# Kernel tuning notes

Measured on AMD Instinct MI355X. Metric: run time of the kernel, lower is better.

The kernel has to match this reference:

```python
import jax, jax.numpy as jnp
import numpy as np

B, T, C = 2, 512, 256
HID = 4 * C
EPS = 1e-5

def _ln(z, g, b):
    mu = z.mean(-1, keepdims=True)
    var = z.var(-1, keepdims=True)
    return (z - mu) / jnp.sqrt(var + EPS) * g + b

def setup_inputs() -> dict:
    key = jax.random.key(0)
    ks = jax.random.split(key, 12)
    s = 0.02
    return {
        'x':   jax.random.normal(ks[0], (B, T, C), dtype=jnp.float32),
        'Wt':  jax.random.normal(ks[1], (C * C, C), dtype=jnp.float32) * s,   # transformation weight (no bias)
        'Wp':  jax.random.normal(ks[2], (C, C), dtype=jnp.float32) * s,       # proj weight
        'bp':  jnp.zeros((C,), dtype=jnp.float32),
        'g1':  jnp.ones((C,), dtype=jnp.float32),
        'b1':  jnp.zeros((C,), dtype=jnp.float32),
        'g2':  jnp.ones((C,), dtype=jnp.float32),
        'b2':  jnp.zeros((C,), dtype=jnp.float32),
        'W1':  jax.random.normal(ks[3], (HID, C), dtype=jnp.float32) * s,     # ffwd first linear
        'bf1': jnp.zeros((HID,), dtype=jnp.float32),
        'W2':  jax.random.normal(ks[4], (C, HID), dtype=jnp.float32) * s,     # ffwd second linear
        'bf2': jnp.zeros((C,), dtype=jnp.float32),
    }

def reference(x, Wt, Wp, bp, g1, b1, g2, b2, W1, bf1, W2, bf2):
    Bs, Ts, Cs = x.shape
    # ---- self-attention branch (pre-LN) ----
    h = _ln(x, g1, b1)
    # transformation: (B,T,C) @ (C, C^2) -> (B,T,C,C); faithfully multiplied by 0 as in source
    transform = (h @ Wt.T).reshape(Bs, Ts, Cs, Cs) * 0.0
    # einsum 'bcij,btj->btcj': contract over i (dim of size C)
    out = jnp.einsum('bcij,btj->btcj', transform, h)  # (B,T,T,C)
    tril = jnp.tril(jnp.ones((Ts, Ts), dtype=bool))
    out = jnp.where(tril[None, :, :, None], out, 0.0)
    out = out.sum(axis=2)  # (B,T,C)
    sa = out @ Wp.T + bp   # proj (dropout=0.0 -> identity)
    x = x + sa
    # ---- feed-forward branch (pre-LN) ----
    h2 = _ln(x, g2, b2)
    ff = jax.nn.relu(h2 @ W1.T + bf1) @ W2.T + bf2
    return x + ff
```

## Files before the change

kernel.cpp:

```cpp
#include <hip/hip_runtime.h>


typedef short bf8_t __attribute__((ext_vector_type(8)));
typedef float f4_t  __attribute__((ext_vector_type(4)));

__device__ inline unsigned short f2bf(float f) {
  unsigned u = __float_as_uint(f);
  u += 0x7fffu + ((u >> 16) & 1u);
  return (unsigned short)(u >> 16);
}

__global__ __launch_bounds__(256) void prep_kernel(
    const float* __restrict__ x, const float* __restrict__ bp,
    const float* __restrict__ g2, const float* __restrict__ b2,
    const float* __restrict__ W1, const float* __restrict__ W2,
    float* __restrict__ xp, unsigned short* __restrict__ h2,
    unsigned short* __restrict__ w1b, unsigned short* __restrict__ w2b) {
  const int b = blockIdx.x, t = threadIdx.x;
  if (b < 1024) {
    const int idx = (b << 8) + t;
    float v = x[idx] + bp[t];
    float s = v, s2 = v * v;
    #pragma unroll
    for (int off = 32; off > 0; off >>= 1) {
      s  += __shfl_down(s, off);
      s2 += __shfl_down(s2, off);
    }
    __shared__ float red[8];
    const int wave = t >> 6, lane = t & 63;
    if (lane == 0) { red[wave] = s; red[4 + wave] = s2; }
    __syncthreads();
    const float ts  = red[0] + red[1] + red[2] + red[3];
    const float ts2 = red[4] + red[5] + red[6] + red[7];
    const float mu   = ts * (1.0f / 256.0f);
    const float var  = ts2 * (1.0f / 256.0f) - mu * mu;
    const float rstd = rsqrtf(var + 1e-5f);
    xp[idx] = v;
    h2[idx] = f2bf((v - mu) * rstd * g2[t] + b2[t]);
  } else {
    const int e = ((b - 1024) << 10) + (t << 2);
    const float* src; unsigned short* dst;
    if (e < 262144) { src = W1 + e;          dst = w1b + e; }
    else            { src = W2 + (e - 262144); dst = w2b + (e - 262144); }
    const float4 v = *(const float4*)src;
    ushort4 o;
    o.x = f2bf(v.x); o.y = f2bf(v.y); o.z = f2bf(v.z); o.w = f2bf(v.w);
    *(ushort4*)dst = o;
  }
}

__global__ __launch_bounds__(256) void gemm1_kernel(
    const unsigned short* __restrict__ A,
    const unsigned short* __restrict__ Bm,
    const float* __restrict__ bias,
    unsigned short* __restrict__ H) {
  __shared__ unsigned short As[64 * 136];
  __shared__ unsigned short Bs[64 * 136];
  const int tid = threadIdx.x;
  const int bm = blockIdx.y << 6, bn = blockIdx.x << 6;
  const int wave = tid >> 6, lane = tid & 63;
  const int wy = (wave >> 1) << 5, wx = (wave & 1) << 5;
  const int quad = lane >> 4, l16 = lane & 15;
  f4_t acc[2][2] = {};

  for (int kt = 0; kt < 256; kt += 128) {
    #pragma unroll
    for (int c = 0; c < 4; ++c) {
      const int ch = (c << 8) + tid;
      const int r = ch >> 4, cc = ch & 15;
      *(uint4*)&As[r * 136 + (cc << 3)] =
          *(const uint4*)&A[((bm + r) << 8) + kt + (cc << 3)];
      *(uint4*)&Bs[r * 136 + (cc << 3)] =
          *(const uint4*)&Bm[((bn + r) << 8) + kt + (cc << 3)];
    }
    __syncthreads();
    #pragma unroll
    for (int ks = 0; ks < 4; ++ks) {
      bf8_t af[2], bv[2];
      #pragma unroll
      for (int i = 0; i < 2; ++i)
        af[i] = *(const bf8_t*)&As[(wy + (i << 4) + l16) * 136 + (ks << 5) + (quad << 3)];
      #pragma unroll
      for (int j = 0; j < 2; ++j)
        bv[j] = *(const bf8_t*)&Bs[(wx + (j << 4) + l16) * 136 + (ks << 5) + (quad << 3)];
      #pragma unroll
      for (int i = 0; i < 2; ++i)
        #pragma unroll
        for (int j = 0; j < 2; ++j)
          acc[i][j] = __builtin_amdgcn_mfma_f32_16x16x32_bf16(af[i], bv[j], acc[i][j], 0, 0, 0);
    }
    __syncthreads();
  }

  #pragma unroll
  for (int j = 0; j < 2; ++j) {
    const int n = bn + wx + (j << 4) + l16;
    const float bvv = bias[n];
    #pragma unroll
    for (int i = 0; i < 2; ++i) {
      #pragma unroll
      for (int r = 0; r < 4; ++r) {
        const int m = bm + wy + (i << 4) + (quad << 2) + r;
        float v = acc[i][j][r] + bvv;
        v = fmaxf(v, 0.0f);
        H[(m << 10) + n] = f2bf(v);
      }
    }
  }
}

__global__ __launch_bounds__(256) void gemm2_kernel(
    const unsigned short* __restrict__ A,
    const unsigned short* __restrict__ Bm,
    const float* __restrict__ bias,
    const float* __restrict__ resid,
    float* __restrict__ out) {
  __shared__ unsigned short As[32 * 264];
  __shared__ unsigned short Bs[32 * 264];
  const int tid = threadIdx.x;
  const int bm = blockIdx.y << 5, bn = blockIdx.x << 5;
  const int wave = tid >> 6, lane = tid & 63;
  const int wy = (wave >> 1) << 4, wx = (wave & 1) << 4;
  const int quad = lane >> 4, l16 = lane & 15;
  f4_t acc = {};

  for (int kt = 0; kt < 1024; kt += 256) {
    #pragma unroll
    for (int c = 0; c < 4; ++c) {
      const int ch = (c << 8) + tid;
      const int r = ch >> 5, cc = ch & 31;
      *(uint4*)&As[r * 264 + (cc << 3)] =
          *(const uint4*)&A[((bm + r) << 10) + kt + (cc << 3)];
      *(uint4*)&Bs[r * 264 + (cc << 3)] =
          *(const uint4*)&Bm[((bn + r) << 10) + kt + (cc << 3)];
    }
    __syncthreads();
    #pragma unroll
    for (int ks = 0; ks < 8; ++ks) {
      const bf8_t af = *(const bf8_t*)&As[(wy + l16) * 264 + (ks << 5) + (quad << 3)];
      const bf8_t bv = *(const bf8_t*)&Bs[(wx + l16) * 264 + (ks << 5) + (quad << 3)];
      acc = __builtin_amdgcn_mfma_f32_16x16x32_bf16(af, bv, acc, 0, 0, 0);
    }
    __syncthreads();
  }

  const int n = bn + wx + l16;
  const float bvv = bias[n];
  #pragma unroll
  for (int r = 0; r < 4; ++r) {
    const int m = bm + wy + (quad << 2) + r;
    out[(m << 8) + n] = acc[r] + bvv + resid[(m << 8) + n];
  }
}

extern "C" void kernel_launch(void* const* d_in, const int* in_sizes, int n_in,
                              void* d_out, int out_size, void* d_ws, size_t ws_size,
                              hipStream_t stream) {
  const float* x   = (const float*)d_in[0];
  const float* bp  = (const float*)d_in[3];
  const float* g2  = (const float*)d_in[6];
  const float* b2  = (const float*)d_in[7];
  const float* W1  = (const float*)d_in[8];
  const float* bf1 = (const float*)d_in[9];
  const float* W2  = (const float*)d_in[10];
  const float* bf2 = (const float*)d_in[11];
  float* out = (float*)d_out;

  float* xp = (float*)d_ws;
  unsigned short* h2  = (unsigned short*)(xp + 262144);
  unsigned short* w1b = h2 + 262144;
  unsigned short* w2b = w1b + 262144;
  unsigned short* H   = w2b + 262144;

  prep_kernel<<<1536, 256, 0, stream>>>(x, bp, g2, b2, W1, W2, xp, h2, w1b, w2b);
  gemm1_kernel<<<dim3(16, 16), 256, 0, stream>>>(h2, w1b, bf1, H);
  gemm2_kernel<<<dim3(8, 32), 256, 0, stream>>>(H, w2b, bf2, xp, out);
}
```

Before: 120.7 us.

## Fuse LayerNorm and weight conversion into first GEMM, drop prep kernel

Removes the separate prep kernel. The first GEMM block now computes LayerNorm of its 64 rows directly into shared memory, converts its W1 tile from fp32 to bf16 in place, and converts a slice of W2 to bf16 for the second GEMM. The second GEMM recomputes the residual from x+bp instead of reading a stored xp, and uses a larger K tile (512) so it needs fewer sync iterations. This saves one launch and the workspace round-trips, but each of the 16 column blocks redundantly recomputes LayerNorm for its row tile, and shared memory use grows.

```diff
diff --git a/kernel.cpp b/kernel.cpp
--- a/kernel.cpp
+++ b/kernel.cpp
@@ -2,7 +2,8 @@
 
 
 typedef short bf8_t __attribute__((ext_vector_type(8)));
-typedef float f4_t  __attribute__((ext_vector_type(4)));
+typedef unsigned short us8_t __attribute__((ext_vector_type(8)));
+typedef float f4_t __attribute__((ext_vector_type(4)));
 
 __device__ inline unsigned short f2bf(float f) {
   unsigned u = __float_as_uint(f);
@@ -10,146 +11,150 @@
   return (unsigned short)(u >> 16);
 }
 
-__global__ __launch_bounds__(256) void prep_kernel(
-    const float* __restrict__ x, const float* __restrict__ bp,
+__global__ __launch_bounds__(256) void k1_kernel(
+    const float* __restrict__ x,  const float* __restrict__ bp,
     const float* __restrict__ g2, const float* __restrict__ b2,
-    const float* __restrict__ W1, const float* __restrict__ W2,
-    float* __restrict__ xp, unsigned short* __restrict__ h2,
-    unsigned short* __restrict__ w1b, unsigned short* __restrict__ w2b) {
-  const int b = blockIdx.x, t = threadIdx.x;
-  if (b < 1024) {
-    const int idx = (b << 8) + t;
-    float v = x[idx] + bp[t];
-    float s = v, s2 = v * v;
+    const float* __restrict__ W1, const float* __restrict__ bf1,
+    const float* __restrict__ W2, unsigned short* __restrict__ w2b,
+    unsigned short* __restrict__ H) {
+  __shared__ unsigned short As[64 * 264];
+  __shared__ unsigned short Bs[64 * 264];
+  const int tid = threadIdx.x;
+  const int bm = (int)blockIdx.y << 6, bn = (int)blockIdx.x << 6;
+  const int wave = tid >> 6, lane = tid & 63;
+
+  #pragma unroll
+  for (int c = 0; c < 8; ++c) {
+    const int ch = (c << 8) + tid;
+    const int r = ch >> 5, cc = ch & 31;
+    const float4 v0 = *(const float4*)&W1[((bn + r) << 8) + (cc << 3)];
+    const float4 v1 = *(const float4*)&W1[((bn + r) << 8) + (cc << 3) + 4];
+    us8_t o;
+    o[0] = f2bf(v0.x); o[1] = f2bf(v0.y); o[2] = f2bf(v0.z); o[3] = f2bf(v0.w);
+    o[4] = f2bf(v1.x); o[5] = f2bf(v1.y); o[6] = f2bf(v1.z); o[7] = f2bf(v1.w);
+    *(us8_t*)&Bs[r * 264 + (cc << 3)] = o;
+  }
+
+  {
+    const float4 bp4 = *(const float4*)&bp[lane << 2];
+    const float4 g4  = *(const float4*)&g2[lane << 2];
+    const float4 b4  = *(const float4*)&b2[lane << 2];
     #pragma unroll
-    for (int off = 32; off > 0; off >>= 1) {
-      s  += __shfl_down(s, off);
-      s2 += __shfl_down(s2, off);
+    for (int half = 0; half < 2; ++half) {
+      float4 xv[8];
+      #pragma unroll
+      for (int i = 0; i < 8; ++i) {
+        const int r = (wave << 4) + (half << 3) + i;
+        xv[i] = *(const float4*)&x[((bm + r) << 8) + (lane << 2)];
+      }
+      #pragma unroll
+      for (int i = 0; i < 8; ++i) {
+        const int r = (wave << 4) + (half << 3) + i;
+        const float a0 = xv[i].x + bp4.x, a1 = xv[i].y + bp4.y;
+        const float a2 = xv[i].z + bp4.z, a3 = xv[i].w + bp4.w;
+        float s  = a0 + a1 + a2 + a3;
+        float s2 = a0 * a0 + a1 * a1 + a2 * a2 + a3 * a3;
+        #pragma unroll
+        for (int off = 32; off > 0; off >>= 1) {
+          s  += __shfl_xor(s, off);
+          s2 += __shfl_xor(s2, off);
+        }
+        const float mu   = s * (1.0f / 256.0f);
+        const float rstd = rsqrtf(s2 * (1.0f / 256.0f) - mu * mu + 1e-5f);
+        ushort4 o;
+        o.x = f2bf((a0 - mu) * rstd * g4.x + b4.x);
+        o.y = f2bf((a1 - mu) * rstd * g4.y + b4.y);
+        o.z = f2bf((a2 - mu) * rstd * g4.z + b4.z);
+        o.w = f2bf((a3 - mu) * rstd * g4.w + b4.w);
+        *(ushort4*)&As[r * 264 + (lane << 2)] = o;
+      }
     }
-    __shared__ float red[8];
-    const int wave = t >> 6, lane = t & 63;
-    if (lane == 0) { red[wave] = s; red[4 + wave] = s2; }
-    __syncthreads();
-    const float ts  = red[0] + red[1] + red[2] + red[3];
-    const float ts2 = red[4] + red[5] + red[6] + red[7];
-    const float mu   = ts * (1.0f / 256.0f);
-    const float var  = ts2 * (1.0f / 256.0f) - mu * mu;
-    const float rstd = rsqrtf(var + 1e-5f);
-    xp[idx] = v;
-    h2[idx] = f2bf((v - mu) * rstd * g2[t] + b2[t]);
-  } else {
-    const int e = ((b - 1024) << 10) + (t << 2);
-    const float* src; unsigned short* dst;
-    if (e < 262144) { src = W1 + e;          dst = w1b + e; }
-    else            { src = W2 + (e - 262144); dst = w2b + (e - 262144); }
-    const float4 v = *(const float4*)src;
-    ushort4 o;
-    o.x = f2bf(v.x); o.y = f2bf(v.y); o.z = f2bf(v.z); o.w = f2bf(v.w);
-    *(ushort4*)dst = o;
   }
-}
 
-__global__ __launch_bounds__(256) void gemm1_kernel(
-    const unsigned short* __restrict__ A,
-    const unsigned short* __restrict__ Bm,
-    const float* __restrict__ bias,
-    unsigned short* __restrict__ H) {
-  __shared__ unsigned short As[64 * 136];
-  __shared__ unsigned short Bs[64 * 136];
-  const int tid = threadIdx.x;
-  const int bm = blockIdx.y << 6, bn = blockIdx.x << 6;
-  const int wave = tid >> 6, lane = tid & 63;
+  {
+    const int base = ((((int)blockIdx.y << 4) + (int)blockIdx.x) << 10) + (tid << 2);
+    const float4 v = *(const float4*)&W2[base];
+    ushort4 o; o.x = f2bf(v.x); o.y = f2bf(v.y); o.z = f2bf(v.z); o.w = f2bf(v.w);
+    *(ushort4*)&w2b[base] = o;
+  }
+
+  __syncthreads();
+
   const int wy = (wave >> 1) << 5, wx = (wave & 1) << 5;
   const int quad = lane >> 4, l16 = lane & 15;
   f4_t acc[2][2] = {};
-
-  for (int kt = 0; kt < 256; kt += 128) {
+  #pragma unroll
+  for (int ks = 0; ks < 8; ++ks) {
+    bf8_t af[2], bv[2];
     #pragma unroll
-    for (int c = 0; c < 4; ++c) {
-      const int ch = (c << 8) + tid;
-      const int r = ch >> 4, cc = ch & 15;
-      *(uint4*)&As[r * 136 + (cc << 3)] =
-          *(const uint4*)&A[((bm + r) << 8) + kt + (cc << 3)];
-      *(uint4*)&Bs[r * 136 + (cc << 3)] =
-          *(const uint4*)&Bm[((bn + r) << 8) + kt + (cc << 3)];
-    }
-    __syncthreads();
+    for (int i = 0; i < 2; ++i)
+      af[i] = *(const bf8_t*)&As[(wy + (i << 4) + l16) * 264 + (ks << 5) + (quad << 3)];
     #pragma unroll
-    for (int ks = 0; ks < 4; ++ks) {
-      bf8_t af[2], bv[2];
-      #pragma unroll
-      for (int i = 0; i < 2; ++i)
-        af[i] = *(const bf8_t*)&As[(wy + (i << 4) + l16) * 136 + (ks << 5) + (quad << 3)];
+    for (int j = 0; j < 2; ++j)
+      bv[j] = *(const bf8_t*)&Bs[(wx + (j << 4) + l16) * 264 + (ks << 5) + (quad << 3)];
+    #pragma unroll
+    for (int i = 0; i < 2; ++i)
       #pragma unroll
       for (int j = 0; j < 2; ++j)
-        bv[j] = *(const bf8_t*)&Bs[(wx + (j << 4) + l16) * 136 + (ks << 5) + (quad << 3)];
-      #pragma unroll
-      for (int i = 0; i < 2; ++i)
-        #pragma unroll
-        for (int j = 0; j < 2; ++j)
-          acc[i][j] = __builtin_amdgcn_mfma_f32_16x16x32_bf16(af[i], bv[j], acc[i][j], 0, 0, 0);
-    }
-    __syncthreads();
+        acc[i][j] = __builtin_amdgcn_mfma_f32_16x16x32_bf16(af[i], bv[j], acc[i][j], 0, 0, 0);
   }
 
   #pragma unroll
   for (int j = 0; j < 2; ++j) {
     const int n = bn + wx + (j << 4) + l16;
-    const float bvv = bias[n];
+    const float bvv = bf1[n];
     #pragma unroll
-    for (int i = 0; i < 2; ++i) {
+    for (int i = 0; i < 2; ++i)
       #pragma unroll
       for (int r = 0; r < 4; ++r) {
         const int m = bm + wy + (i << 4) + (quad << 2) + r;
-        float v = acc[i][j][r] + bvv;
-        v = fmaxf(v, 0.0f);
-        H[(m << 10) + n] = f2bf(v);
+        H[(m << 10) + n] = f2bf(fmaxf(acc[i][j][r] + bvv, 0.0f));
       }
-    }
   }
 }
 
-__global__ __launch_bounds__(256) void gemm2_kernel(
+__global__ __launch_bounds__(256) void k2_kernel(
     const unsigned short* __restrict__ A,
     const unsigned short* __restrict__ Bm,
-    const float* __restrict__ bias,
-    const float* __restrict__ resid,
+    const float* __restrict__ bf2,
+    const float* __restrict__ x, const float* __restrict__ bp,
     float* __restrict__ out) {
-  __shared__ unsigned short As[32 * 264];
-  __shared__ unsigned short Bs[32 * 264];
+  __shared__ unsigned short As[32 * 520];
+  __shared__ unsigned short Bs[32 * 520];
   const int tid = threadIdx.x;
-  const int bm = blockIdx.y << 5, bn = blockIdx.x << 5;
+  const int bm = (int)blockIdx.y << 5, bn = (int)blockIdx.x << 5;
   const int wave = tid >> 6, lane = tid & 63;
   const int wy = (wave >> 1) << 4, wx = (wave & 1) << 4;
   const int quad = lane >> 4, l16 = lane & 15;
   f4_t acc = {};
 
-  for (int kt = 0; kt < 1024; kt += 256) {
+  for (int kt = 0; kt < 1024; kt += 512) {
     #pragma unroll
-    for (int c = 0; c < 4; ++c) {
+    for (int c = 0; c < 8; ++c) {
       const int ch = (c << 8) + tid;
-      const int r = ch >> 5, cc = ch & 31;
-      *(uint4*)&As[r * 264 + (cc << 3)] =
+      const int r = ch >> 6, cc = ch & 63;
+      *(uint4*)&As[r * 520 + (cc << 3)] =
           *(const uint4*)&A[((bm + r) << 10) + kt + (cc << 3)];
-      *(uint4*)&Bs[r * 264 + (cc << 3)] =
+      *(uint4*)&Bs[r * 520 + (cc << 3)] =
           *(const uint4*)&Bm[((bn + r) << 10) + kt + (cc << 3)];
     }
     __syncthreads();
     #pragma unroll
-    for (int ks = 0; ks < 8; ++ks) {
-      const bf8_t af = *(const bf8_t*)&As[(wy + l16) * 264 + (ks << 5) + (quad << 3)];
-      const bf8_t bv = *(const bf8_t*)&Bs[(wx + l16) * 264 + (ks << 5) + (quad << 3)];
+    for (int ks = 0; ks < 16; ++ks) {
+      const bf8_t af = *(const bf8_t*)&As[(wy + l16) * 520 + (ks << 5) + (quad << 3)];
+      const bf8_t bv = *(const bf8_t*)&Bs[(wx + l16) * 520 + (ks << 5) + (quad << 3)];
       acc = __builtin_amdgcn_mfma_f32_16x16x32_bf16(af, bv, acc, 0, 0, 0);
     }
     __syncthreads();
   }
 
   const int n = bn + wx + l16;
-  const float bvv = bias[n];
+  const float bvv = bf2[n];
+  const float bpn = bp[n];
   #pragma unroll
   for (int r = 0; r < 4; ++r) {
     const int m = bm + wy + (quad << 2) + r;
-    out[(m << 8) + n] = acc[r] + bvv + resid[(m << 8) + n];
+    out[(m << 8) + n] = acc[r] + bvv + x[(m << 8) + n] + bpn;
   }
 }
 
@@ -166,13 +171,9 @@
   const float* bf2 = (const float*)d_in[11];
   float* out = (float*)d_out;
 
-  float* xp = (float*)d_ws;
-  unsigned short* h2  = (unsigned short*)(xp + 262144);
-  unsigned short* w1b = h2 + 262144;
-  unsigned short* w2b = w1b + 262144;
+  unsigned short* w2b = (unsigned short*)d_ws;
   unsigned short* H   = w2b + 262144;
 
-  prep_kernel<<<1536, 256, 0, stream>>>(x, bp, g2, b2, W1, W2, xp, h2, w1b, w2b);
-  gemm1_kernel<<<dim3(16, 16), 256, 0, stream>>>(h2, w1b, bf1, H);
-  gemm2_kernel<<<dim3(8, 32), 256, 0, stream>>>(H, w2b, bf2, xp, out);
+  k1_kernel<<<dim3(16, 16), 256, 0, stream>>>(x, bp, g2, b2, W1, bf1, W2, w2b, H);
+  k2_kernel<<<dim3(8, 32), 256, 0, stream>>>(H, w2b, bf2, x, bp, out);
 }
```

After: 122.6 us. No clear change (+1.5%).
